# Optimization experiments

Measured on AMD Instinct MI355X. Metric: run time of the kernel, lower is better.

The kernel has to match this reference:

```python
import jax, jax.numpy as jnp
import numpy as np

B, T, H, POOL, MAX_ITER = 32, 1024, 128, 16, 4
D = 2 * H  # feature size of U rows


def _maxout(x, w, b, out_dim, pool):
    # x: [..., fin], w: [fin, out_dim*pool], b: [out_dim*pool]
    y = x @ w + b
    y = y.reshape(y.shape[:-1] + (out_dim, pool))
    return y.max(axis=-1)


def _hmn(U, us, ue, h, WDw, WDb, W1w, W1b, W2w, W2b, W3w, W3b):
    # U: [B,T,2H]; us, ue: [B,2H]; h: [B,H] -> scores [B,T]
    r = jnp.tanh(jnp.concatenate([h, us, ue], axis=-1) @ WDw + WDb)  # [B,H]
    rt = jnp.broadcast_to(r[:, None, :], (U.shape[0], U.shape[1], r.shape[-1]))
    m1 = _maxout(jnp.concatenate([U, rt], axis=-1), W1w, W1b, H, POOL)  # [B,T,H]
    m2 = _maxout(m1, W2w, W2b, H, POOL)                                  # [B,T,H]
    m3 = _maxout(jnp.concatenate([m1, m2], axis=-1), W3w, W3b, 1, POOL)  # [B,T,1]
    return m3[..., 0]  # [B,T]


def _lstm_cell(x, h, c, wih, whh, bih, bhh):
    gates = x @ wih.T + bih + h @ whh.T + bhh  # [B,4H]
    i, f, g, o = jnp.split(gates, 4, axis=-1)
    i, f, o = jax.nn.sigmoid(i), jax.nn.sigmoid(f), jax.nn.sigmoid(o)
    g = jnp.tanh(g)
    c2 = f * c + i * g
    h2 = o * jnp.tanh(c2)
    return h2, c2


def setup_inputs() -> dict:
    key = jax.random.key(0)
    ks = jax.random.split(key, 24)
    s = 0.05
    gn = lambda k, shape: (jax.random.normal(k, shape, jnp.float32) * s)
    inp = {"U": jax.random.normal(ks[0], (B, T, D), jnp.float32)}
    for tag, off in (("s", 1), ("e", 9)):
        inp[f"WD{tag}_w"] = gn(ks[off + 0], (5 * H, H))
        inp[f"WD{tag}_b"] = jnp.zeros((H,), jnp.float32)
        inp[f"W1{tag}_w"] = gn(ks[off + 1], (3 * H, H * POOL))
        inp[f"W1{tag}_b"] = jnp.zeros((H * POOL,), jnp.float32)
        inp[f"W2{tag}_w"] = gn(ks[off + 2], (H, H * POOL))
        inp[f"W2{tag}_b"] = jnp.zeros((H * POOL,), jnp.float32)
        inp[f"W3{tag}_w"] = gn(ks[off + 3], (2 * H, POOL))
        inp[f"W3{tag}_b"] = jnp.zeros((POOL,), jnp.float32)
    inp["lstm_wih"] = gn(ks[20], (4 * H, 4 * H))
    inp["lstm_whh"] = gn(ks[21], (4 * H, H))
    inp["lstm_bih"] = jnp.zeros((4 * H,), jnp.float32)
    inp["lstm_bhh"] = jnp.zeros((4 * H,), jnp.float32)
    return inp


def reference(U,
              WDs_w, WDs_b, W1s_w, W1s_b, W2s_w, W2s_b, W3s_w, W3s_b,
              WDe_w, WDe_b, W1e_w, W1e_b, W2e_w, W2e_b, W3e_w, W3e_b,
              lstm_wih, lstm_whh, lstm_bih, lstm_bhh):
    b = U.shape[0]
    bidx = jnp.arange(b)
    h = jnp.zeros((b, H), U.dtype)
    c = jnp.zeros((b, H), U.dtype)
    us, ue = U[:, 0, :], U[:, 1, :]
    entropies = []
    for _ in range(MAX_ITER):  # training-mode: run all iterations (no host-sync early stop)
        alpha_sc = _hmn(U, us, ue, h, WDs_w, WDs_b, W1s_w, W1s_b, W2s_w, W2s_b, W3s_w, W3s_b)
        alpha = jnp.argmax(alpha_sc, axis=1)           # [B]
        us = U[bidx, alpha, :]                          # data-dependent gather
        beta_sc = _hmn(U, us, ue, h, WDe_w, WDe_b, W1e_w, W1e_b, W2e_w, W2e_b, W3e_w, W3e_b)
        beta = jnp.argmax(beta_sc, axis=1)
        ue = U[bidx, beta, :]
        h, c = _lstm_cell(jnp.concatenate([us, ue], axis=1), h, c,
                          lstm_wih, lstm_whh, lstm_bih, lstm_bhh)
        entropies.append(jnp.stack([alpha_sc, beta_sc], axis=0))
    ent = jnp.stack(entropies, axis=0)  # [max_iter, 2, B, T]
    return alpha, beta, ent
```

## Files before the change

kernel.cpp:

```cpp
#include <hip/hip_runtime.h>
#include <math.h>

static constexpr int cB = 32;
static constexpr int cT = 1024;
static constexpr int cH = 128;
static constexpr int cD = 256;
static constexpr int cN = 2048;
static constexpr int cM = cB * cT;

typedef __attribute__((ext_vector_type(8))) short short8;
typedef __attribute__((ext_vector_type(4))) float f32x4;

__device__ __forceinline__ ushort f2bf(float x) {
    union { float f; unsigned u; } v; v.f = x;
    unsigned r = v.u + 0x7FFF + ((v.u >> 16) & 1);
    return (ushort)(r >> 16);
}
__device__ __forceinline__ float bf2f(ushort h) {
    union { float f; unsigned u; } v; v.u = ((unsigned)h) << 16;
    return v.f;
}

__device__ __forceinline__ void gload_lds16(const ushort* g, ushort* l) {
    __builtin_amdgcn_global_load_lds(
        (const __attribute__((address_space(1))) unsigned int*)(const void*)g,
        (__attribute__((address_space(3))) unsigned int*)(void*)l,
        16, 0, 0);
}

template<int K, bool WRITE_HL>
__global__ __launch_bounds__(256, 2)
void mfma_pool_swp(const ushort* __restrict__ Wth, const ushort* __restrict__ Wtl,
                   const ushort* __restrict__ Xh, const ushort* __restrict__ Xl,
                   const float* __restrict__ initv, int init_bstride,
                   float* __restrict__ out, ushort* __restrict__ outh,
                   ushort* __restrict__ outl)
{
    constexpr int KH = K / 128;
    __shared__ __attribute__((aligned(16))) ushort sWh[128 * 128];
    __shared__ __attribute__((aligned(16))) ushort sWl[128 * 128];

    const int tid  = threadIdx.x;
    const int wave = tid >> 6;
    const int lane = tid & 63;
    const int l15  = lane & 15;
    const int lg   = lane >> 4;
    const int wr   = wave >> 1;
    const int wc   = wave & 1;

    const int wg  = blockIdx.x;
    const int lin = (wg & 7) * 512 + (wg >> 3);
    const int bx  = lin & 15;
    const int by  = lin >> 4;
    const int n0  = bx * 128;
    const int m0  = by * 128;
    const size_t ibase = (size_t)(m0 >> 10) * init_bstride;

    float ivv[4][4];
    #pragma unroll
    for (int rf = 0; rf < 4; ++rf)
        #pragma unroll
        for (int r = 0; r < 4; ++r)
            ivv[rf][r] = initv[ibase + n0 + wr * 64 + rf * 16 + lg * 4 + r];

    f32x4 acc[4][4];
    #pragma unroll
    for (int rf = 0; rf < 4; ++rf)
        #pragma unroll
        for (int cf = 0; cf < 4; ++cf)
            acc[rf][cf] = (f32x4){0.f, 0.f, 0.f, 0.f};

    const int st_row_lo = lane >> 4;
    const int st_slot   = lane & 15;

    #pragma unroll
    for (int kh = 0; kh < KH; ++kh) {
        const int kb = kh * 128;
        if (kh > 0) __syncthreads();

        #pragma unroll
        for (int j = 0; j < 8; ++j) {
            int i   = wave * 8 + j;
            int row = i * 4 + st_row_lo;
            int ck  = st_slot ^ (row & 7);
            size_t goff = (size_t)(n0 + row) * K + kb + ck * 8;
            gload_lds16(Wth + goff, sWh + i * 512);
            gload_lds16(Wtl + goff, sWl + i * 512);
        }
        short8 xh_[16], xl_[16];
        #pragma unroll
        for (int cf = 0; cf < 4; ++cf)
            #pragma unroll
            for (int ks = 0; ks < 4; ++ks) {
                size_t off = (size_t)(m0 + wc * 64 + cf * 16 + l15) * K
                           + kb + ks * 32 + lg * 8;
                xh_[cf * 4 + ks] = *(const short8*)(Xh + off);
                xl_[cf * 4 + ks] = *(const short8*)(Xl + off);
            }
        __syncthreads();

        #pragma unroll
        for (int ks = 0; ks < 4; ++ks) {
            short8 w_h[4], w_l[4];
            #pragma unroll
            for (int rf = 0; rf < 4; ++rf) {
                int row  = wr * 64 + rf * 16 + l15;
                int ck2  = ks * 4 + lg;
                int adr  = row * 128 + ((ck2 ^ (row & 7)) * 8);
                w_h[rf] = *(const short8*)(sWh + adr);
                w_l[rf] = *(const short8*)(sWl + adr);
            }
            #pragma unroll
            for (int rf = 0; rf < 4; ++rf)
                #pragma unroll
                for (int cf = 0; cf < 4; ++cf) {
                    acc[rf][cf] = __builtin_amdgcn_mfma_f32_16x16x32_bf16(
                        w_h[rf], xh_[cf * 4 + ks], acc[rf][cf], 0, 0, 0);
                    acc[rf][cf] = __builtin_amdgcn_mfma_f32_16x16x32_bf16(
                        w_l[rf], xh_[cf * 4 + ks], acc[rf][cf], 0, 0, 0);
                    acc[rf][cf] = __builtin_amdgcn_mfma_f32_16x16x32_bf16(
                        w_h[rf], xl_[cf * 4 + ks], acc[rf][cf], 0, 0, 0);
                }
        }
    }

    const int NP = 128;
    #pragma unroll
    for (int rf = 0; rf < 4; ++rf) {
        const int o2 = (n0 >> 4) + wr * 4 + rf;
        #pragma unroll
        for (int cf = 0; cf < 4; ++cf) {
            float v0 = acc[rf][cf][0] + ivv[rf][0];
            float v1 = acc[rf][cf][1] + ivv[rf][1];
            float v2 = acc[rf][cf][2] + ivv[rf][2];
            float v3 = acc[rf][cf][3] + ivv[rf][3];
            float mx = fmaxf(fmaxf(v0, v1), fmaxf(v2, v3));
            mx = fmaxf(mx, __shfl_xor(mx, 16));
            mx = fmaxf(mx, __shfl_xor(mx, 32));
            if (lane < 16) {
                int m = m0 + wc * 64 + cf * 16 + lane;
                size_t o = (size_t)m * NP + o2;
                out[o] = mx;
                if (WRITE_HL) {
                    ushort hb = f2bf(mx);
                    outh[o] = hb;
                    outl[o] = f2bf(mx - bf2f(hb));
                }
            }
        }
    }
}

__global__ __launch_bounds__(256, 2)
void mfma_gemm_a1(const ushort* __restrict__ Uh, const ushort* __restrict__ Ul,
                  const ushort* __restrict__ Bth, const ushort* __restrict__ Btl,
                  float* __restrict__ out)
{
    constexpr int K = 256;
    __shared__ __attribute__((aligned(16))) ushort sBh[128 * 128];
    __shared__ __attribute__((aligned(16))) ushort sBl[128 * 128];

    const int tid  = threadIdx.x;
    const int wave = tid >> 6;
    const int lane = tid & 63;
    const int l15  = lane & 15;
    const int lg   = lane >> 4;
    const int wr   = wave >> 1;
    const int wc   = wave & 1;

    const int wg  = blockIdx.x;
    const int lin = (wg & 7) * 512 + (wg >> 3);
    const int bx  = lin & 15;
    const int by  = lin >> 4;
    const int n0  = bx * 128;
    const int m0  = by * 128;

    f32x4 acc[4][4];
    #pragma unroll
    for (int mf = 0; mf < 4; ++mf)
        #pragma unroll
        for (int nf = 0; nf < 4; ++nf)
            acc[mf][nf] = (f32x4){0.f, 0.f, 0.f, 0.f};

    const int st_row_lo = lane >> 4;
    const int st_slot   = lane & 15;

    #pragma unroll
    for (int kh = 0; kh < 2; ++kh) {
        const int kb = kh * 128;
        if (kh > 0) __syncthreads();

        #pragma unroll
        for (int j = 0; j < 8; ++j) {
            int i   = wave * 8 + j;
            int row = i * 4 + st_row_lo;
            int ck  = st_slot ^ (row & 7);
            size_t goff = (size_t)(n0 + row) * K + kb + ck * 8;
            gload_lds16(Bth + goff, sBh + i * 512);
            gload_lds16(Btl + goff, sBl + i * 512);
        }
        short8 ph[16], pl[16];
        #pragma unroll
        for (int mf = 0; mf < 4; ++mf)
            #pragma unroll
            for (int ks = 0; ks < 4; ++ks) {
                size_t off = (size_t)(m0 + wr * 64 + mf * 16 + l15) * K
                           + kb + ks * 32 + lg * 8;
                ph[mf * 4 + ks] = *(const short8*)(Uh + off);
                pl[mf * 4 + ks] = *(const short8*)(Ul + off);
            }
        __syncthreads();

        #pragma unroll
        for (int ks = 0; ks < 4; ++ks) {
            short8 b_h[4], b_l[4];
            #pragma unroll
            for (int nf = 0; nf < 4; ++nf) {
                int row  = wc * 64 + nf * 16 + l15;
                int ck2  = ks * 4 + lg;
                int adr  = row * 128 + ((ck2 ^ (row & 7)) * 8);
                b_h[nf] = *(const short8*)(sBh + adr);
                b_l[nf] = *(const short8*)(sBl + adr);
            }
            #pragma unroll
            for (int mf = 0; mf < 4; ++mf)
                #pragma unroll
                for (int nf = 0; nf < 4; ++nf) {
                    acc[mf][nf] = __builtin_amdgcn_mfma_f32_16x16x32_bf16(
                        ph[mf * 4 + ks], b_h[nf], acc[mf][nf], 0, 0, 0);
                    acc[mf][nf] = __builtin_amdgcn_mfma_f32_16x16x32_bf16(
                        ph[mf * 4 + ks], b_l[nf], acc[mf][nf], 0, 0, 0);
                    acc[mf][nf] = __builtin_amdgcn_mfma_f32_16x16x32_bf16(
                        pl[mf * 4 + ks], b_h[nf], acc[mf][nf], 0, 0, 0);
                }
        }
    }

    #pragma unroll
    for (int mf = 0; mf < 4; ++mf)
        #pragma unroll
        for (int nf = 0; nf < 4; ++nf) {
            int col = n0 + wc * 64 + nf * 16 + l15;
            #pragma unroll
            for (int r = 0; r < 4; ++r) {
                int row = m0 + wr * 64 + mf * 16 + lg * 4 + r;
                out[(size_t)row * cN + col] = acc[mf][nf][r];
            }
        }
}

__global__ void m1_from_a1_kernel(const float* __restrict__ A1,
                                  const float* __restrict__ rterm,
                                  float* __restrict__ m1,
                                  ushort* __restrict__ m1h,
                                  ushort* __restrict__ m1l)
{
    int idx = blockIdx.x * 256 + threadIdx.x;
    int m = idx >> 7;
    int o = idx & 127;
    int b = m >> 10;
    const float4* a  = (const float4*)(A1 + (size_t)m * cN + o * 16);
    const float4* rt = (const float4*)(rterm + (size_t)b * cN + o * 16);
    float mx = -3.4e38f;
    #pragma unroll
    for (int q = 0; q < 4; ++q) {
        float4 av = a[q];
        float4 rv = rt[q];
        mx = fmaxf(mx, fmaxf(fmaxf(av.x + rv.x, av.y + rv.y),
                             fmaxf(av.z + rv.z, av.w + rv.w)));
    }
    m1[idx] = mx;
    ushort hb = f2bf(mx);
    m1h[idx] = hb;
    m1l[idx] = f2bf(mx - bf2f(hb));
}

__global__ void wsplit_kernel(const float* __restrict__ W, int K, int N,
                              ushort* __restrict__ th, ushort* __restrict__ tl)
{
    int idx = blockIdx.x * 256 + threadIdx.x;
    if (idx >= K * N) return;
    int k = idx / N, n = idx - k * N;
    float x = W[idx];
    ushort h = f2bf(x);
    th[(size_t)n * K + k] = h;
    tl[(size_t)n * K + k] = f2bf(x - bf2f(h));
}

__global__ void usplit_kernel(const float* __restrict__ U,
                              ushort* __restrict__ uh, ushort* __restrict__ ul)
{
    int idx = blockIdx.x * 256 + threadIdx.x;
    float x = U[idx];
    ushort h = f2bf(x);
    uh[idx] = h;
    ul[idx] = f2bf(x - bf2f(h));
}

__global__ void r_kernel(const float* __restrict__ h, const float* __restrict__ us,
                         const float* __restrict__ ue,
                         const float* __restrict__ WDw, const float* __restrict__ WDb,
                         float* __restrict__ r)
{
    int b = blockIdx.x;
    int j = threadIdx.x;
    __shared__ float x[640];
    x[j]       = h[b * cH + j];
    x[128 + j] = us[b * cD + j];
    x[256 + j] = us[b * cD + 128 + j];
    x[384 + j] = ue[b * cD + j];
    x[512 + j] = ue[b * cD + 128 + j];
    __syncthreads();
    float s = WDb[j];
    for (int k = 0; k < 640; ++k) s = fmaf(x[k], WDw[(size_t)k * cH + j], s);
    r[b * cH + j] = tanhf(s);
}

__global__ void rterm_kernel(const float* __restrict__ r, const float* __restrict__ W1r,
                             const float* __restrict__ W1b, float* __restrict__ rterm)
{
    int b = blockIdx.y;
    int n = blockIdx.x * 256 + threadIdx.x;
    __shared__ float rs[128];
    if (threadIdx.x < 128) rs[threadIdx.x] = r[b * cH + threadIdx.x];
    __syncthreads();
    float s = W1b[n];
    for (int k = 0; k < 128; ++k) s = fmaf(rs[k], W1r[(size_t)k * cN + n], s);
    rterm[(size_t)b * cN + n] = s;
}

__global__ __launch_bounds__(256)
void score_kernel(const float* __restrict__ m1, const float* __restrict__ m2,
                  const float* __restrict__ W3w, const float* __restrict__ W3b,
                  float* __restrict__ ent)
{
    __shared__ float xs[16][257];
    __shared__ float wsh[256 * 16];
    int tid = threadIdx.x;
    int m0 = blockIdx.x * 16;
    #pragma unroll
    for (int q = 0; q < 16; ++q) wsh[tid + q * 256] = W3w[tid + q * 256];
    #pragma unroll
    for (int q = 0; q < 8; ++q) {
        int f = tid + q * 256;
        int rl = f >> 7, col = f & 127;
        xs[rl][col]       = m1[(size_t)(m0 + rl) * cH + col];
        xs[rl][128 + col] = m2[(size_t)(m0 + rl) * cH + col];
    }
    __syncthreads();
    int rl = tid >> 4, p = tid & 15;
    float s = W3b[p];
    for (int k = 0; k < 256; ++k) s = fmaf(xs[rl][k], wsh[k * 16 + p], s);
    #pragma unroll
    for (int off = 8; off; off >>= 1) s = fmaxf(s, __shfl_xor(s, off));
    if (p == 0) ent[m0 + rl] = s;
}

__global__ void argmax_kernel(const float* __restrict__ sc, const float* __restrict__ U,
                              float* __restrict__ uvec, float* __restrict__ outidx)
{
    int b = blockIdx.x;
    int tid = threadIdx.x;
    float bv = -3.4e38f;
    int bi = 0x7fffffff;
    for (int t = tid; t < cT; t += 256) {
        float v = sc[b * cT + t];
        if (v > bv || (v == bv && t < bi)) { bv = v; bi = t; }
    }
    __shared__ float vs[256];
    __shared__ int   is[256];
    vs[tid] = bv; is[tid] = bi;
    __syncthreads();
    for (int s = 128; s > 0; s >>= 1) {
        if (tid < s) {
            if (vs[tid + s] > vs[tid] ||
                (vs[tid + s] == vs[tid] && is[tid + s] < is[tid])) {
                vs[tid] = vs[tid + s];
                is[tid] = is[tid + s];
            }
        }
        __syncthreads();
    }
    int best = is[0];
    if (tid == 0) outidx[b] = (float)best;
    uvec[b * cD + tid % cD] = U[((size_t)b * cT + best) * cD + (tid % cD)];
}

__global__ void lstm_kernel(const float* __restrict__ us, const float* __restrict__ ue,
                            float* __restrict__ h, float* __restrict__ c,
                            const float* __restrict__ wih, const float* __restrict__ whh,
                            const float* __restrict__ bih, const float* __restrict__ bhh)
{
    int b = blockIdx.x;
    int j = threadIdx.x;
    __shared__ float x[512];
    __shared__ float hh[128];
    x[j]       = us[b * cD + j];
    x[128 + j] = us[b * cD + 128 + j];
    x[256 + j] = ue[b * cD + j];
    x[384 + j] = ue[b * cD + 128 + j];
    hh[j] = h[b * cH + j];
    __syncthreads();
    float g4[4];
    #pragma unroll
    for (int gi = 0; gi < 4; ++gi) {
        int row = gi * 128 + j;
        float s = bih[row] + bhh[row];
        const float* wr = wih + (size_t)row * 512;
        for (int k = 0; k < 512; ++k) s = fmaf(x[k], wr[k], s);
        const float* wr2 = whh + (size_t)row * 128;
        for (int k = 0; k < 128; ++k) s = fmaf(hh[k], wr2[k], s);
        g4[gi] = s;
    }
    float i_ = 1.f / (1.f + expf(-g4[0]));
    float f_ = 1.f / (1.f + expf(-g4[1]));
    float g_ = tanhf(g4[2]);
    float o_ = 1.f / (1.f + expf(-g4[3]));
    float c2 = f_ * c[b * cH + j] + i_ * g_;
    float h2 = o_ * tanhf(c2);
    c[b * cH + j] = c2;
    h[b * cH + j] = h2;
}

__global__ void init_kernel(const float* __restrict__ U, float* __restrict__ us,
                            float* __restrict__ ue, float* __restrict__ h,
                            float* __restrict__ c)
{
    int i = blockIdx.x * 256 + threadIdx.x;
    if (i < cB * cD) {
        int b = i >> 8, d = i & 255;
        us[i] = U[((size_t)b * cT + 0) * cD + d];
        ue[i] = U[((size_t)b * cT + 1) * cD + d];
    }
    if (i < cB * cH) { h[i] = 0.f; c[i] = 0.f; }
}

extern "C" void kernel_launch(void* const* d_in, const int* in_sizes, int n_in,
                              void* d_out, int out_size, void* d_ws, size_t ws_size,
                              hipStream_t stream)
{
    const float* U = (const float*)d_in[0];
    const float* WD_w[2] = {(const float*)d_in[1], (const float*)d_in[9]};
    const float* WD_b[2] = {(const float*)d_in[2], (const float*)d_in[10]};
    const float* W1_w[2] = {(const float*)d_in[3], (const float*)d_in[11]};
    const float* W1_b[2] = {(const float*)d_in[4], (const float*)d_in[12]};
    const float* W2_w[2] = {(const float*)d_in[5], (const float*)d_in[13]};
    const float* W2_b[2] = {(const float*)d_in[6], (const float*)d_in[14]};
    const float* W3_w[2] = {(const float*)d_in[7], (const float*)d_in[15]};
    const float* W3_b[2] = {(const float*)d_in[8], (const float*)d_in[16]};
    const float* wih = (const float*)d_in[17];
    const float* whh = (const float*)d_in[18];
    const float* bih = (const float*)d_in[19];
    const float* bhh = (const float*)d_in[20];

    float* ws = (float*)d_ws;
    float* m1 = ws;
    float* m2 = m1 + (size_t)cM * cH;
    float* us = m2 + (size_t)cM * cH;
    float* ue = us + cB * cD;
    float* h  = ue + cB * cD;
    float* c  = h + cB * cH;
    float* r  = c + cB * cH;
    float* rterm = r + cB * cH;
    float* cur = rterm + (size_t)cB * cN;

    ushort* m1h = (ushort*)cur;                   cur += (size_t)cM * cH / 2;
    ushort* m1l = (ushort*)cur;                   cur += (size_t)cM * cH / 2;
    ushort* Uh  = (ushort*)cur;                   cur += (size_t)cM * cD / 2;
    ushort* Ul  = (ushort*)cur;                   cur += (size_t)cM * cD / 2;
    ushort* W1th[2], *W1tl[2], *W2th[2], *W2tl[2];
    for (int sd = 0; sd < 2; ++sd) {
        W1th[sd] = (ushort*)cur; cur += (size_t)cN * cD / 2;
        W1tl[sd] = (ushort*)cur; cur += (size_t)cN * cD / 2;
        W2th[sd] = (ushort*)cur; cur += (size_t)cN * cH / 2;
        W2tl[sd] = (ushort*)cur; cur += (size_t)cN * cH / 2;
    }
    float* A1[2];
    A1[0] = cur;
    A1[1] = A1[0] + (size_t)cM * cN;

    size_t baseFloats = (size_t)(A1[0] - ws);
    int preN = 0;
    if (ws_size >= (baseFloats + 2 * (size_t)cM * cN) * sizeof(float)) preN = 2;
    else if (ws_size >= (baseFloats + (size_t)cM * cN) * sizeof(float)) preN = 1;

    float* outf = (float*)d_out;

    init_kernel<<<32, 256, 0, stream>>>(U, us, ue, h, c);
    usplit_kernel<<<(cM * cD) / 256, 256, 0, stream>>>(U, Uh, Ul);
    for (int sd = 0; sd < 2; ++sd) {
        wsplit_kernel<<<(cD * cN) / 256, 256, 0, stream>>>(
            W1_w[sd], cD, cN, W1th[sd], W1tl[sd]);
        wsplit_kernel<<<(cH * cN) / 256, 256, 0, stream>>>(
            W2_w[sd], cH, cN, W2th[sd], W2tl[sd]);
    }

    const int ggrid = (cN / 128) * (cM / 128);
    for (int sd = 0; sd < preN; ++sd)
        mfma_gemm_a1<<<ggrid, 256, 0, stream>>>(
            Uh, Ul, W1th[sd], W1tl[sd], A1[sd]);

    for (int it = 0; it < 4; ++it) {
        for (int sd = 0; sd < 2; ++sd) {
            r_kernel<<<32, 128, 0, stream>>>(h, us, ue, WD_w[sd], WD_b[sd], r);
            rterm_kernel<<<dim3(8, 32), 256, 0, stream>>>(
                r, W1_w[sd] + (size_t)256 * cN, W1_b[sd], rterm);
            if (sd < preN) {
                m1_from_a1_kernel<<<16384, 256, 0, stream>>>(
                    A1[sd], rterm, m1, m1h, m1l);
            } else {
                mfma_pool_swp<256, true><<<ggrid, 256, 0, stream>>>(
                    W1th[sd], W1tl[sd], Uh, Ul, rterm, cN, m1, m1h, m1l);
            }
            mfma_pool_swp<128, false><<<ggrid, 256, 0, stream>>>(
                W2th[sd], W2tl[sd], m1h, m1l, W2_b[sd], 0, m2, nullptr, nullptr);
            float* ent = outf + 64 + (size_t)(it * 2 + sd) * cB * cT;
            score_kernel<<<2048, 256, 0, stream>>>(m1, m2, W3_w[sd], W3_b[sd], ent);
            argmax_kernel<<<32, 256, 0, stream>>>(ent, U, sd ? ue : us,
                                                  outf + (sd ? 32 : 0));
        }
        lstm_kernel<<<32, 128, 0, stream>>>(us, ue, h, c, wih, whh, bih, bhh);
    }
}
```

Measured before the change: 2.864 ms.

## Drop precomputed U·W1 GEMM path and add weight-stationary m2 maxout kernel

Removes the up-front U·W1 GEMM cache (A1 buffers) and the m1_from_a1 kernel, so every iteration recomputes layer 1 with the fused pool kernel. This avoids writing and re-reading two 256 MB fp32 A1 buffers. The layer-2 maxout now uses a new kernel that loads each 128x128 weight tile into LDS once and loops over four 128-row M-chunks, cutting the weight reloads and the block count by four. The trade-off is more MFMA work per iteration for layer 1 and fewer blocks in flight for layer 2.

```diff
diff --git a/kernel.cpp b/kernel.cpp
--- a/kernel.cpp
+++ b/kernel.cpp
@@ -26,6 +26,117 @@
         (const __attribute__((address_space(1))) unsigned int*)(const void*)g,
         (__attribute__((address_space(3))) unsigned int*)(void*)l,
         16, 0, 0);
+}
+
+__global__ __launch_bounds__(256, 2)
+void mfma_pool_m2(const ushort* __restrict__ Wth, const ushort* __restrict__ Wtl,
+                  const ushort* __restrict__ Xh, const ushort* __restrict__ Xl,
+                  const float* __restrict__ bias, float* __restrict__ out)
+{
+    constexpr int K = 128, S = 4;
+    __shared__ __attribute__((aligned(16))) ushort sWh[128 * 128];
+    __shared__ __attribute__((aligned(16))) ushort sWl[128 * 128];
+
+    const int tid  = threadIdx.x;
+    const int wave = tid >> 6;
+    const int lane = tid & 63;
+    const int l15  = lane & 15;
+    const int lg   = lane >> 4;
+    const int wr   = wave >> 1;
+    const int wc   = wave & 1;
+
+    const int wg  = blockIdx.x;
+    const int lin = (wg & 7) * 128 + (wg >> 3);
+    const int bx  = lin & 15;
+    const int by  = lin >> 4;
+    const int n0  = bx * 128;
+
+    float ivv[4][4];
+    #pragma unroll
+    for (int rf = 0; rf < 4; ++rf)
+        #pragma unroll
+        for (int r = 0; r < 4; ++r)
+            ivv[rf][r] = bias[n0 + wr * 64 + rf * 16 + lg * 4 + r];
+
+    const int st_row_lo = lane >> 4;
+    const int st_slot   = lane & 15;
+    #pragma unroll
+    for (int j = 0; j < 8; ++j) {
+        int i   = wave * 8 + j;
+        int row = i * 4 + st_row_lo;
+        int ck  = st_slot ^ (row & 7);
+        size_t goff = (size_t)(n0 + row) * K + ck * 8;
+        gload_lds16(Wth + goff, sWh + i * 512);
+        gload_lds16(Wtl + goff, sWl + i * 512);
+    }
+    __syncthreads();
+
+    const int NP = 128;
+    #pragma unroll
+    for (int s = 0; s < S; ++s) {
+        const int m0 = by * 512 + s * 128;
+
+        short8 xh_[16], xl_[16];
+        #pragma unroll
+        for (int cf = 0; cf < 4; ++cf)
+            #pragma unroll
+            for (int ks = 0; ks < 4; ++ks) {
+                size_t off = (size_t)(m0 + wc * 64 + cf * 16 + l15) * K
+                           + ks * 32 + lg * 8;
+                xh_[cf * 4 + ks] = *(const short8*)(Xh + off);
+                xl_[cf * 4 + ks] = *(const short8*)(Xl + off);
+            }
+
+        f32x4 acc[4][4];
+        #pragma unroll
+        for (int rf = 0; rf < 4; ++rf)
+            #pragma unroll
+            for (int cf = 0; cf < 4; ++cf)
+                acc[rf][cf] = (f32x4){0.f, 0.f, 0.f, 0.f};
+
+        #pragma unroll
+        for (int ks = 0; ks < 4; ++ks) {
+            short8 w_h[4], w_l[4];
+            #pragma unroll
+            for (int rf = 0; rf < 4; ++rf) {
+                int row  = wr * 64 + rf * 16 + l15;
+                int ck2  = ks * 4 + lg;
+                int adr  = row * 128 + ((ck2 ^ (row & 7)) * 8);
+                w_h[rf] = *(const short8*)(sWh + adr);
+                w_l[rf] = *(const short8*)(sWl + adr);
+            }
+            #pragma unroll
+            for (int rf = 0; rf < 4; ++rf)
+                #pragma unroll
+                for (int cf = 0; cf < 4; ++cf) {
+                    acc[rf][cf] = __builtin_amdgcn_mfma_f32_16x16x32_bf16(
+                        w_h[rf], xh_[cf * 4 + ks], acc[rf][cf], 0, 0, 0);
+                    acc[rf][cf] = __builtin_amdgcn_mfma_f32_16x16x32_bf16(
+                        w_l[rf], xh_[cf * 4 + ks], acc[rf][cf], 0, 0, 0);
+                    acc[rf][cf] = __builtin_amdgcn_mfma_f32_16x16x32_bf16(
+                        w_h[rf], xl_[cf * 4 + ks], acc[rf][cf], 0, 0, 0);
+                }
+        }
+
+        #pragma unroll
+        for (int rf = 0; rf < 4; ++rf) {
+            const int o2 = (n0 >> 4) + wr * 4 + rf;
+            #pragma unroll
+            for (int cf = 0; cf < 4; ++cf) {
+                float v0 = acc[rf][cf][0] + ivv[rf][0];
+                float v1 = acc[rf][cf][1] + ivv[rf][1];
+                float v2 = acc[rf][cf][2] + ivv[rf][2];
+                float v3 = acc[rf][cf][3] + ivv[rf][3];
+                float mx = fmaxf(fmaxf(v0, v1), fmaxf(v2, v3));
+                mx = fmaxf(mx, __shfl_xor(mx, 16));
+                mx = fmaxf(mx, __shfl_xor(mx, 32));
+                if (lane < 16) {
+                    int m = m0 + wc * 64 + cf * 16 + lane;
+                    out[(size_t)m * NP + o2] = mx;
+                }
+            }
+        }
+    }
 }
 
 template<int K, bool WRITE_HL>
@@ -151,130 +262,6 @@
     }
 }
 
-__global__ __launch_bounds__(256, 2)
-void mfma_gemm_a1(const ushort* __restrict__ Uh, const ushort* __restrict__ Ul,
-                  const ushort* __restrict__ Bth, const ushort* __restrict__ Btl,
-                  float* __restrict__ out)
-{
-    constexpr int K = 256;
-    __shared__ __attribute__((aligned(16))) ushort sBh[128 * 128];
-    __shared__ __attribute__((aligned(16))) ushort sBl[128 * 128];
-
-    const int tid  = threadIdx.x;
-    const int wave = tid >> 6;
-    const int lane = tid & 63;
-    const int l15  = lane & 15;
-    const int lg   = lane >> 4;
-    const int wr   = wave >> 1;
-    const int wc   = wave & 1;
-
-    const int wg  = blockIdx.x;
-    const int lin = (wg & 7) * 512 + (wg >> 3);
-    const int bx  = lin & 15;
-    const int by  = lin >> 4;
-    const int n0  = bx * 128;
-    const int m0  = by * 128;
-
-    f32x4 acc[4][4];
-    #pragma unroll
-    for (int mf = 0; mf < 4; ++mf)
-        #pragma unroll
-        for (int nf = 0; nf < 4; ++nf)
-            acc[mf][nf] = (f32x4){0.f, 0.f, 0.f, 0.f};
-
-    const int st_row_lo = lane >> 4;
-    const int st_slot   = lane & 15;
-
-    #pragma unroll
-    for (int kh = 0; kh < 2; ++kh) {
-        const int kb = kh * 128;
-        if (kh > 0) __syncthreads();
-
-        #pragma unroll
-        for (int j = 0; j < 8; ++j) {
-            int i   = wave * 8 + j;
-            int row = i * 4 + st_row_lo;
-            int ck  = st_slot ^ (row & 7);
-            size_t goff = (size_t)(n0 + row) * K + kb + ck * 8;
-            gload_lds16(Bth + goff, sBh + i * 512);
-            gload_lds16(Btl + goff, sBl + i * 512);
-        }
-        short8 ph[16], pl[16];
-        #pragma unroll
-        for (int mf = 0; mf < 4; ++mf)
-            #pragma unroll
-            for (int ks = 0; ks < 4; ++ks) {
-                size_t off = (size_t)(m0 + wr * 64 + mf * 16 + l15) * K
-                           + kb + ks * 32 + lg * 8;
-                ph[mf * 4 + ks] = *(const short8*)(Uh + off);
-                pl[mf * 4 + ks] = *(const short8*)(Ul + off);
-            }
-        __syncthreads();
-
-        #pragma unroll
-        for (int ks = 0; ks < 4; ++ks) {
-            short8 b_h[4], b_l[4];
-            #pragma unroll
-            for (int nf = 0; nf < 4; ++nf) {
-                int row  = wc * 64 + nf * 16 + l15;
-                int ck2  = ks * 4 + lg;
-                int adr  = row * 128 + ((ck2 ^ (row & 7)) * 8);
-                b_h[nf] = *(const short8*)(sBh + adr);
-                b_l[nf] = *(const short8*)(sBl + adr);
-            }
-            #pragma unroll
-            for (int mf = 0; mf < 4; ++mf)
-                #pragma unroll
-                for (int nf = 0; nf < 4; ++nf) {
-                    acc[mf][nf] = __builtin_amdgcn_mfma_f32_16x16x32_bf16(
-                        ph[mf * 4 + ks], b_h[nf], acc[mf][nf], 0, 0, 0);
-                    acc[mf][nf] = __builtin_amdgcn_mfma_f32_16x16x32_bf16(
-                        ph[mf * 4 + ks], b_l[nf], acc[mf][nf], 0, 0, 0);
-                    acc[mf][nf] = __builtin_amdgcn_mfma_f32_16x16x32_bf16(
-                        pl[mf * 4 + ks], b_h[nf], acc[mf][nf], 0, 0, 0);
-                }
-        }
-    }
-
-    #pragma unroll
-    for (int mf = 0; mf < 4; ++mf)
-        #pragma unroll
-        for (int nf = 0; nf < 4; ++nf) {
-            int col = n0 + wc * 64 + nf * 16 + l15;
-            #pragma unroll
-            for (int r = 0; r < 4; ++r) {
-                int row = m0 + wr * 64 + mf * 16 + lg * 4 + r;
-                out[(size_t)row * cN + col] = acc[mf][nf][r];
-            }
-        }
-}
-
-__global__ void m1_from_a1_kernel(const float* __restrict__ A1,
-                                  const float* __restrict__ rterm,
-                                  float* __restrict__ m1,
-                                  ushort* __restrict__ m1h,
-                                  ushort* __restrict__ m1l)
-{
-    int idx = blockIdx.x * 256 + threadIdx.x;
-    int m = idx >> 7;
-    int o = idx & 127;
-    int b = m >> 10;
-    const float4* a  = (const float4*)(A1 + (size_t)m * cN + o * 16);
-    const float4* rt = (const float4*)(rterm + (size_t)b * cN + o * 16);
-    float mx = -3.4e38f;
-    #pragma unroll
-    for (int q = 0; q < 4; ++q) {
-        float4 av = a[q];
-        float4 rv = rt[q];
-        mx = fmaxf(mx, fmaxf(fmaxf(av.x + rv.x, av.y + rv.y),
-                             fmaxf(av.z + rv.z, av.w + rv.w)));
-    }
-    m1[idx] = mx;
-    ushort hb = f2bf(mx);
-    m1h[idx] = hb;
-    m1l[idx] = f2bf(mx - bf2f(hb));
-}
-
 __global__ void wsplit_kernel(const float* __restrict__ W, int K, int N,
                               ushort* __restrict__ th, ushort* __restrict__ tl)
 {
@@ -475,14 +462,6 @@
         W2th[sd] = (ushort*)cur; cur += (size_t)cN * cH / 2;
         W2tl[sd] = (ushort*)cur; cur += (size_t)cN * cH / 2;
     }
-    float* A1[2];
-    A1[0] = cur;
-    A1[1] = A1[0] + (size_t)cM * cN;
-
-    size_t baseFloats = (size_t)(A1[0] - ws);
-    int preN = 0;
-    if (ws_size >= (baseFloats + 2 * (size_t)cM * cN) * sizeof(float)) preN = 2;
-    else if (ws_size >= (baseFloats + (size_t)cM * cN) * sizeof(float)) preN = 1;
 
     float* outf = (float*)d_out;
 
@@ -496,24 +475,15 @@
     }
 
     const int ggrid = (cN / 128) * (cM / 128);
-    for (int sd = 0; sd < preN; ++sd)
-        mfma_gemm_a1<<<ggrid, 256, 0, stream>>>(
-            Uh, Ul, W1th[sd], W1tl[sd], A1[sd]);
-
     for (int it = 0; it < 4; ++it) {
         for (int sd = 0; sd < 2; ++sd) {
             r_kernel<<<32, 128, 0, stream>>>(h, us, ue, WD_w[sd], WD_b[sd], r);
             rterm_kernel<<<dim3(8, 32), 256, 0, stream>>>(
                 r, W1_w[sd] + (size_t)256 * cN, W1_b[sd], rterm);
-            if (sd < preN) {
-                m1_from_a1_kernel<<<16384, 256, 0, stream>>>(
-                    A1[sd], rterm, m1, m1h, m1l);
-            } else {
-                mfma_pool_swp<256, true><<<ggrid, 256, 0, stream>>>(
-                    W1th[sd], W1tl[sd], Uh, Ul, rterm, cN, m1, m1h, m1l);
-            }
-            mfma_pool_swp<128, false><<<ggrid, 256, 0, stream>>>(
-                W2th[sd], W2tl[sd], m1h, m1l, W2_b[sd], 0, m2, nullptr, nullptr);
+            mfma_pool_swp<256, true><<<ggrid, 256, 0, stream>>>(
+                W1th[sd], W1tl[sd], Uh, Ul, rterm, cN, m1, m1h, m1l);
+            mfma_pool_m2<<<1024, 256, 0, stream>>>(
+                W2th[sd], W2tl[sd], m1h, m1l, W2_b[sd], m2);
             float* ent = outf + 64 + (size_t)(it * 2 + sd) * cB * cT;
             score_kernel<<<2048, 256, 0, stream>>>(m1, m2, W3_w[sd], W3_b[sd], ent);
             argmax_kernel<<<32, 256, 0, stream>>>(ent, U, sd ? ue : us,
```

Measured after the change: 2.802 ms. 2.1% less time.
